# Kernel tuning notes

Hardware: AMD Instinct MI355X
Metric: run time of the kernel (lower is better)

The kernel has to match this reference:

```python
import jax, jax.numpy as jnp
import numpy as np

N = 50000        # num nodes
E = 1600000      # num edges (avg degree 32)
DIN = 128        # dim_in
DOUT = 256       # dim_out
DA = 32          # dim_atten
SLOPE = 0.2      # leaky_relu negative slope


def setup_inputs() -> dict:
    key = jax.random.key(0)
    ks = jax.random.split(key, 9)
    x = jax.random.normal(ks[0], (N, DIN), dtype=jnp.float32)
    row = jax.random.randint(ks[1], (E,), 0, N, dtype=jnp.int32)
    col = jax.random.randint(ks[2], (E,), 0, N, dtype=jnp.int32)
    adj_val = jax.random.uniform(ks[3], (E,), dtype=jnp.float32)
    # learned params (Linear weights stored as [in, out] for x @ W)
    W_row = (jax.random.normal(ks[4], (DIN, DA)) / np.sqrt(DIN)).astype(jnp.float32)
    W_col = (jax.random.normal(ks[5], (DIN, DA)) / np.sqrt(DIN)).astype(jnp.float32)
    W_x = (jax.random.normal(ks[6], (DIN, DOUT)) / np.sqrt(DIN)).astype(jnp.float32)
    b_x = jnp.zeros((DOUT,), dtype=jnp.float32)
    return {"x": x, "row": row, "col": col, "adj_val": adj_val,
            "W_row": W_row, "W_col": W_col, "W_x": W_x, "b_x": b_x}


def reference(x, row, col, adj_val, W_row, W_col, W_x, b_x):
    # per-node attention projections
    a_row = x @ W_row                      # [N, DA]
    a_col = x @ W_col                      # [N, DA]
    # 'Multiply' attention: per-edge dot product scaled by rsqrt(DA)
    atten = jnp.sum(a_row[row] * a_col[col], axis=1) * jax.lax.rsqrt(jnp.float32(DA))  # [E]
    atten = jnp.where(atten >= 0, atten, SLOPE * atten)   # leaky_relu
    atten = jnp.exp(atten - jnp.max(atten))               # global-max-shifted exp
    # row-sum normalization (segment softmax denominator)
    deg = jax.ops.segment_sum(atten, row, num_segments=N)  # [N]
    atten = atten * (1.0 / (deg + 1e-15))[row]             # [E]
    # atten_combine == 'plus': average with original adjacency values
    vals = (adj_val + atten) * 0.5                         # [E]
    # sparse-dense matmul: out[i] = sum_{e: row[e]==i} vals[e] * x[col[e]]
    out = jax.ops.segment_sum(vals[:, None] * x[col], row, num_segments=N)  # [N, DIN]
    return out @ W_x + b_x                                 # [N, DOUT]
```

## Files before the change

kernel.cpp:

```cpp
#include <hip/hip_runtime.h>


#define DIN   128
#define DOUT  256
#define DA    32
#define SLOPE 0.2f
#define RSQRT_DA 0.17677669529663687f
#define BSH   7
#define NBMAX 512
#define BH_CHUNK 8192
#define PB_CHUNK 8192

typedef unsigned int uint;
typedef unsigned short ushort;
typedef __attribute__((ext_vector_type(8))) short bf16x8;
typedef __attribute__((ext_vector_type(4))) float f32x4;

static __device__ __forceinline__ ushort f2bf(float f) {
  const uint u = __float_as_uint(f);
  return (ushort)((u + 0x7fffu + ((u >> 16) & 1u)) >> 16);
}

__global__ __launch_bounds__(256) void wconv_kernel(
    const float* __restrict__ Wx, ushort* __restrict__ wxt,
    const float* __restrict__ Wr, const float* __restrict__ Wc,
    ushort* __restrict__ wrct, int* __restrict__ bcnt, int nb) {
  __shared__ ushort s[16][DIN];
  const int t = threadIdx.x;
  const int b = blockIdx.x;
  if (b < 16) {
    const int c0 = b * 16;
#pragma unroll
    for (int u = 0; u < 8; ++u) {
      const int k = u * 16 + (t >> 4);
      s[t & 15][k] = f2bf(Wx[(size_t)k * DOUT + c0 + (t & 15)]);
    }
    __syncthreads();
    const int c = t >> 4;
    const int kk = (t & 15) * 8;
    *(uint4*)(wxt + (size_t)(c0 + c) * DIN + kk) = *(const uint4*)&s[c][kk];
  } else if (b < 20) {
    const int c = (b - 16) * 16 + (t >> 4);
    const int k0 = (t & 15) * 8;
    const float* src = (c < DA) ? (Wr + c) : (Wc + (c - DA));
    ushort h[8];
#pragma unroll
    for (int j = 0; j < 8; ++j) h[j] = f2bf(src[(size_t)(k0 + j) * DA]);
    uint4 v;
    v.x = (uint)h[0] | ((uint)h[1] << 16);
    v.y = (uint)h[2] | ((uint)h[3] << 16);
    v.z = (uint)h[4] | ((uint)h[5] << 16);
    v.w = (uint)h[6] | ((uint)h[7] << 16);
    *(uint4*)(wrct + (size_t)c * DIN + k0) = v;
  } else {
    for (int i = t; i < nb; i += 256) bcnt[i] = 0;
  }
}

__global__ __launch_bounds__(256) void proj_kernel(
    const float* __restrict__ x, const ushort* __restrict__ wrct,
    float* __restrict__ a_row, ushort* __restrict__ a_colh,
    ushort* __restrict__ xh) {
  __shared__ ushort xb[16][136];
  const int t = threadIdx.x;
  const int node0 = blockIdx.x * 16;
  const float4* xg = (const float4*)(x + (size_t)node0 * DIN);
#pragma unroll
  for (int u = 0; u < 2; ++u) {
    const int f = t + u * 256;
    const float4 v = xg[f];
    ushort4 h;
    h.x = f2bf(v.x); h.y = f2bf(v.y); h.z = f2bf(v.z); h.w = f2bf(v.w);
    *(ushort4*)&xb[f >> 5][(f & 31) * 4] = h;
    ((ushort4*)(xh + (size_t)node0 * DIN))[f] = h;
  }
  __syncthreads();

  const int w = t >> 6;
  const int l = t & 63;
  const int lr = l & 15;
  const int lk = (l >> 4) * 8;
  f32x4 acc = {0.f, 0.f, 0.f, 0.f};
#pragma unroll
  for (int kk = 0; kk < 4; ++kk) {
    const bf16x8 a = *(const bf16x8*)&xb[lr][kk * 32 + lk];
    const bf16x8 bb =
        *(const bf16x8*)(wrct + (size_t)(w * 16 + lr) * DIN + kk * 32 + lk);
    acc = __builtin_amdgcn_mfma_f32_16x16x32_bf16(a, bb, acc, 0, 0, 0);
  }
  const int col = w * 16 + lr;
  const int r0 = (l >> 4) * 4;
#pragma unroll
  for (int r = 0; r < 4; ++r) {
    const int node = node0 + r0 + r;
    if (col < DA)
      a_row[(size_t)node * DA + col] = acc[r] * RSQRT_DA;
    else
      a_colh[(size_t)node * DA + (col - DA)] = f2bf(acc[r]);
  }
}

__global__ __launch_bounds__(512) void bhist_kernel(
    const int* __restrict__ row, int* __restrict__ bcnt, int nb, int E) {
  __shared__ int hist[NBMAX];
  const int t = threadIdx.x;
  for (int b = t; b < nb; b += 512) hist[b] = 0;
  __syncthreads();
  const int e0 = blockIdx.x * BH_CHUNK;
  for (int u = 0; u < BH_CHUNK / 512; ++u) {
    const int e = e0 + u * 512 + t;
    if (e < E) atomicAdd(&hist[row[e] >> BSH], 1);
  }
  __syncthreads();
  for (int b = t; b < nb; b += 512) {
    const int c = hist[b];
    if (c) atomicAdd(&bcnt[b], c);
  }
}

__global__ __launch_bounds__(512) void bscan_kernel(
    const int* __restrict__ bcnt, int* __restrict__ bstart,
    int* __restrict__ bcursor, int nb) {
  __shared__ int s[512];
  const int t = threadIdx.x;
  const int v = (t < nb) ? bcnt[t] : 0;
  s[t] = v;
  __syncthreads();
  for (int ofs = 1; ofs < 512; ofs <<= 1) {
    const int tmp = (t >= ofs) ? s[t - ofs] : 0;
    __syncthreads();
    s[t] += tmp;
    __syncthreads();
  }
  if (t < nb) {
    const int ex = s[t] - v;
    bstart[t] = ex;
    bcursor[t] = ex;
  }
  if (t == nb) bstart[nb] = s[nb - 1];
}

__global__ __launch_bounds__(512) void part_kernel(
    const int* __restrict__ row, const int* __restrict__ col,
    const float* __restrict__ adj, int* __restrict__ bcursor,
    int2* __restrict__ ibuf, int nb, int E) {
  __shared__ int hist[NBMAX];
  __shared__ int base[NBMAX];
  const int t = threadIdx.x;
  const int e0 = blockIdx.x * PB_CHUNK;
  for (int b = t; b < nb; b += 512) hist[b] = 0;
  __syncthreads();
  for (int u = 0; u < PB_CHUNK / 512; ++u) {
    const int e = e0 + u * 512 + t;
    if (e < E) atomicAdd(&hist[row[e] >> BSH], 1);
  }
  __syncthreads();
  for (int b = t; b < nb; b += 512) {
    const int c = hist[b];
    base[b] = c ? atomicAdd(&bcursor[b], c) : 0;
    hist[b] = 0;
  }
  __syncthreads();
  for (int u = 0; u < PB_CHUNK / 512; ++u) {
    const int e = e0 + u * 512 + t;
    if (e < E) {
      const int r = row[e];
      const int b = r >> BSH;
      const int pos = base[b] + atomicAdd(&hist[b], 1);
      ibuf[pos] = make_int2(((r & 127) << 16) | col[e], __float_as_int(adj[e]));
    }
  }
}

__global__ __launch_bounds__(512) void csr_kernel(
    const int* __restrict__ bstart, const int2* __restrict__ ibuf,
    int* __restrict__ off, int2* __restrict__ pk, int n, int E) {
  __shared__ int cnt[128];
  __shared__ int excl[128];
  const int b = blockIdx.x;
  const int t = threadIdx.x;
  const int estart = bstart[b];
  const int eend = bstart[b + 1];
  if (t < 128) cnt[t] = 0;
  __syncthreads();
  for (int e = estart + t; e < eend; e += 512)
    atomicAdd(&cnt[ibuf[e].x >> 16], 1);
  __syncthreads();
  if (t < 128) excl[t] = cnt[t];
  __syncthreads();
  for (int ofs = 1; ofs < 128; ofs <<= 1) {
    const int v = (t < 128 && t >= ofs) ? excl[t - ofs] : 0;
    __syncthreads();
    if (t < 128) excl[t] += v;
    __syncthreads();
  }
  if (t < 128) excl[t] -= cnt[t];
  __syncthreads();
  const int node0 = b << BSH;
  if (t < 128 && node0 + t < n) off[node0 + t] = estart + excl[t];
  if (b == gridDim.x - 1 && t == 0) off[n] = E;
  if (t < 128) cnt[t] = 0;
  __syncthreads();
  for (int e = estart + t; e < eend; e += 512) {
    const int2 v = ibuf[e];
    const int rl = v.x >> 16;
    const int pos = estart + excl[rl] + atomicAdd(&cnt[rl], 1);
    pk[pos] = make_int2(v.x & 0xffff, v.y);
  }
}

#define NODE_BODY(J)                                                    \
  {                                                                     \
    const int2 e = spk[w][half][(J)];                                   \
    const float pv = sp[w][half][(J)];                                  \
    const uint2 xv = xh2[(size_t)e.x * 32 + la];                        \
    const float av = __int_as_float(e.y);                               \
    const float f0 = __uint_as_float(xv.x << 16);                       \
    const float f1 = __uint_as_float(xv.x & 0xffff0000u);               \
    const float f2 = __uint_as_float(xv.y << 16);                       \
    const float f3 = __uint_as_float(xv.y & 0xffff0000u);               \
    aa0 += av * f0; aa1 += av * f1; aa2 += av * f2; aa3 += av * f3;     \
    ap0 += pv * f0; ap1 += pv * f1; ap2 += pv * f2; ap3 += pv * f3;     \
    deg += pv;                                                          \
  }

__global__ __launch_bounds__(256) void node_kernel(
    const uint* __restrict__ xh, const float* __restrict__ a_row,
    const ushort* __restrict__ a_colh, const int* __restrict__ off,
    const int2* __restrict__ pk, ushort* __restrict__ feath, int n) {
  __shared__ int2  spk[4][2][32];
  __shared__ float sp[4][2][32];
  __shared__ float s_ar[4][2][32];
  const int t = threadIdx.x;
  const int w = t >> 6;
  const int lane = t & 63;
  const int half = lane >> 5;
  const int la = lane & 31;
  const int i0 = blockIdx.x * 8 + w * 2;
  if (i0 >= n) return;
  const int i = i0 + half;
  s_ar[w][half][la] = (i < n) ? a_row[(size_t)i * DA + la] : 0.f;
  const int o0 = off[i0];
  const int o1 = off[i0 + 1];
  const int o2 = (i0 + 2 <= n) ? off[i0 + 2] : o1;
  const int d0 = o1 - o0, d1 = o2 - o1;
  const int myoff = half ? o1 : o0;
  const int myd = half ? d1 : d0;
  const int dmax = max(d0, d1);
  const uint2* xh2 = (const uint2*)xh;

  float aa0 = 0.f, aa1 = 0.f, aa2 = 0.f, aa3 = 0.f;
  float ap0 = 0.f, ap1 = 0.f, ap2 = 0.f, ap3 = 0.f;
  float deg = 0.f;

  for (int base = 0; base < dmax; base += 32) {
    const int m = myd - base;
    if (la < m) {
      const int2 e = pk[myoff + base + la];
      spk[w][half][la] = e;
      const uint4* ac = (const uint4*)(a_colh + (size_t)e.x * DA);
      const float* ar = s_ar[w][half];
      float dot = 0.f;
#pragma unroll
      for (int k = 0; k < 4; ++k) {
        const uint4 q = ac[k];
        const float* a = ar + k * 8;
        dot += __uint_as_float(q.x << 16) * a[0] +
               __uint_as_float(q.x & 0xffff0000u) * a[1] +
               __uint_as_float(q.y << 16) * a[2] +
               __uint_as_float(q.y & 0xffff0000u) * a[3] +
               __uint_as_float(q.z << 16) * a[4] +
               __uint_as_float(q.z & 0xffff0000u) * a[5] +
               __uint_as_float(q.w << 16) * a[6] +
               __uint_as_float(q.w & 0xffff0000u) * a[7];
      }
      const float lg = (dot >= 0.f) ? dot : SLOPE * dot;
      sp[w][half][la] = __expf(lg);
    } else {
      spk[w][half][la] = make_int2(0, 0);
      sp[w][half][la] = 0.f;
    }
    const int mmax = min(32, dmax - base);
    int j = 0;
    for (; j + 8 <= mmax; j += 8) {
#pragma unroll
      for (int u = 0; u < 8; ++u) NODE_BODY(j + u)
    }
    for (; j < mmax; ++j) NODE_BODY(j)
  }
  if (i < n) {
    const float inv = 0.5f / (deg + 1e-15f);
    ushort4 h;
    h.x = f2bf(0.5f * aa0 + inv * ap0);
    h.y = f2bf(0.5f * aa1 + inv * ap1);
    h.z = f2bf(0.5f * aa2 + inv * ap2);
    h.w = f2bf(0.5f * aa3 + inv * ap3);
    *(ushort4*)(feath + (size_t)i * DIN + la * 4) = h;
  }
}

__global__ __launch_bounds__(256) void gemm_kernel(
    const ushort* __restrict__ feath, const ushort* __restrict__ wxt,
    const float* __restrict__ bx, float* __restrict__ out) {
  const int t = threadIdx.x;
  const int w = t >> 6;
  const int l = t & 63;
  const int row0 = blockIdx.x * 16;
  const int lr = l & 15;
  const int lk = (l >> 4) * 8;
  const int col0 = w * 64;

  f32x4 acc[4] = {f32x4{0.f, 0.f, 0.f, 0.f}, f32x4{0.f, 0.f, 0.f, 0.f},
                  f32x4{0.f, 0.f, 0.f, 0.f}, f32x4{0.f, 0.f, 0.f, 0.f}};
  const ushort* Abase = feath + (size_t)(row0 + lr) * DIN + lk;
#pragma unroll
  for (int kk = 0; kk < 4; ++kk) {
    const bf16x8 a = *(const bf16x8*)(Abase + kk * 32);
#pragma unroll
    for (int ct = 0; ct < 4; ++ct) {
      const bf16x8 b =
          *(const bf16x8*)(wxt + (size_t)(col0 + ct * 16 + lr) * DIN + kk * 32 + lk);
      acc[ct] = __builtin_amdgcn_mfma_f32_16x16x32_bf16(a, b, acc[ct], 0, 0, 0);
    }
  }
  const int crow0 = row0 + (l >> 4) * 4;
#pragma unroll
  for (int ct = 0; ct < 4; ++ct) {
    const int c = col0 + ct * 16 + lr;
    const float bv = bx[c];
#pragma unroll
    for (int r = 0; r < 4; ++r)
      out[(size_t)(crow0 + r) * DOUT + c] = acc[ct][r] + bv;
  }
}

extern "C" void kernel_launch(void* const* d_in, const int* in_sizes, int n_in,
                              void* d_out, int out_size, void* d_ws, size_t ws_size,
                              hipStream_t stream) {
  const float* x   = (const float*)d_in[0];
  const int*   row = (const int*)d_in[1];
  const int*   col = (const int*)d_in[2];
  const float* adj = (const float*)d_in[3];
  const float* Wr  = (const float*)d_in[4];
  const float* Wc  = (const float*)d_in[5];
  const float* Wx  = (const float*)d_in[6];
  const float* bx  = (const float*)d_in[7];
  float* out = (float*)d_out;

  const int n = in_sizes[0] / DIN;
  const int E = in_sizes[1];
  const int nb = (n + 127) >> BSH;

  int* w4 = (int*)d_ws;
  float* a_row   = (float*)w4;  w4 += (size_t)n * DA;
  ushort* feath  = (ushort*)w4; w4 += (size_t)n * DIN / 2;
  int2*  ibuf    = (int2*)feath;
  int*   off     = w4;          w4 += n + 1;
  int*   bcnt    = w4;          w4 += nb;
  int*   bstart  = w4;          w4 += nb + 1;
  int*   bcursor = w4;          w4 += nb;
  w4 = (int*)(((uintptr_t)w4 + 15) & ~(uintptr_t)15);
  ushort* a_colh = (ushort*)w4; w4 += (size_t)n * DA / 2;
  uint*   xh     = (uint*)w4;   w4 += (size_t)n * DIN / 2;
  int2*   pk     = (int2*)w4;   w4 += (size_t)E * 2;
  ushort* wxt    = (ushort*)w4; w4 += (size_t)DOUT * DIN / 2;
  ushort* wrct   = (ushort*)w4;

  wconv_kernel<<<21, 256, 0, stream>>>(Wx, wxt, Wr, Wc, wrct, bcnt, nb);
  proj_kernel<<<n / 16, 256, 0, stream>>>(x, wrct, a_row, a_colh, (ushort*)xh);
  bhist_kernel<<<(E + BH_CHUNK - 1) / BH_CHUNK, 512, 0, stream>>>(row, bcnt, nb, E);
  bscan_kernel<<<1, 512, 0, stream>>>(bcnt, bstart, bcursor, nb);
  part_kernel<<<(E + PB_CHUNK - 1) / PB_CHUNK, 512, 0, stream>>>(
      row, col, adj, bcursor, ibuf, nb, E);
  csr_kernel<<<nb, 512, 0, stream>>>(bstart, ibuf, off, pk, n, E);
  node_kernel<<<(n + 7) / 8, 256, 0, stream>>>(
      (const uint*)xh, a_row, a_colh, off, pk, feath, n);
  gemm_kernel<<<n / 16, 256, 0, stream>>>(feath, wxt, bx, out);
}
```

Baseline: 295.9 us.

## Replace histogram/scan/CSR passes with fixed-capacity buckets and in-block CSR sort

Drops the bucket histogram, scan and CSR-build kernels. Each bucket of 64 rows now gets a fixed slot of 2560 edges, with padded cursors initialised by wconv. The node kernel loads its bucket's edges into shared memory, counting-sorts them by local row, then processes its 64 nodes in a loop. This removes two extra passes over the edge list and several launches. In exchange, any bucket holding more than 2560 edges overflows silently, and the node kernel runs far fewer, larger blocks with more shared memory, which may cut latency hiding for the gathers.

```diff
diff --git a/kernel.cpp b/kernel.cpp
--- a/kernel.cpp
+++ b/kernel.cpp
@@ -6,9 +6,10 @@
 #define DA    32
 #define SLOPE 0.2f
 #define RSQRT_DA 0.17677669529663687f
-#define BSH   7
-#define NBMAX 512
-#define BH_CHUNK 8192
+#define BSH   6
+#define BCAP  2560
+#define CSTRIDE 32
+#define NBMAX 800
 #define PB_CHUNK 8192
 
 typedef unsigned int uint;
@@ -24,7 +25,7 @@
 __global__ __launch_bounds__(256) void wconv_kernel(
     const float* __restrict__ Wx, ushort* __restrict__ wxt,
     const float* __restrict__ Wr, const float* __restrict__ Wc,
-    ushort* __restrict__ wrct, int* __restrict__ bcnt, int nb) {
+    ushort* __restrict__ wrct, int* __restrict__ bcursor, int nb) {
   __shared__ ushort s[16][DIN];
   const int t = threadIdx.x;
   const int b = blockIdx.x;
@@ -53,7 +54,7 @@
     v.w = (uint)h[6] | ((uint)h[7] << 16);
     *(uint4*)(wrct + (size_t)c * DIN + k0) = v;
   } else {
-    for (int i = t; i < nb; i += 256) bcnt[i] = 0;
+    for (int i = t; i < nb; i += 256) bcursor[i * CSTRIDE] = i * BCAP;
   }
 }
 
@@ -100,46 +101,6 @@
   }
 }
 
-__global__ __launch_bounds__(512) void bhist_kernel(
-    const int* __restrict__ row, int* __restrict__ bcnt, int nb, int E) {
-  __shared__ int hist[NBMAX];
-  const int t = threadIdx.x;
-  for (int b = t; b < nb; b += 512) hist[b] = 0;
-  __syncthreads();
-  const int e0 = blockIdx.x * BH_CHUNK;
-  for (int u = 0; u < BH_CHUNK / 512; ++u) {
-    const int e = e0 + u * 512 + t;
-    if (e < E) atomicAdd(&hist[row[e] >> BSH], 1);
-  }
-  __syncthreads();
-  for (int b = t; b < nb; b += 512) {
-    const int c = hist[b];
-    if (c) atomicAdd(&bcnt[b], c);
-  }
-}
-
-__global__ __launch_bounds__(512) void bscan_kernel(
-    const int* __restrict__ bcnt, int* __restrict__ bstart,
-    int* __restrict__ bcursor, int nb) {
-  __shared__ int s[512];
-  const int t = threadIdx.x;
-  const int v = (t < nb) ? bcnt[t] : 0;
-  s[t] = v;
-  __syncthreads();
-  for (int ofs = 1; ofs < 512; ofs <<= 1) {
-    const int tmp = (t >= ofs) ? s[t - ofs] : 0;
-    __syncthreads();
-    s[t] += tmp;
-    __syncthreads();
-  }
-  if (t < nb) {
-    const int ex = s[t] - v;
-    bstart[t] = ex;
-    bcursor[t] = ex;
-  }
-  if (t == nb) bstart[nb] = s[nb - 1];
-}
-
 __global__ __launch_bounds__(512) void part_kernel(
     const int* __restrict__ row, const int* __restrict__ col,
     const float* __restrict__ adj, int* __restrict__ bcursor,
@@ -157,7 +118,7 @@
   __syncthreads();
   for (int b = t; b < nb; b += 512) {
     const int c = hist[b];
-    base[b] = c ? atomicAdd(&bcursor[b], c) : 0;
+    base[b] = c ? atomicAdd(&bcursor[b * CSTRIDE], c) : 0;
     hist[b] = 0;
   }
   __syncthreads();
@@ -167,45 +128,8 @@
       const int r = row[e];
       const int b = r >> BSH;
       const int pos = base[b] + atomicAdd(&hist[b], 1);
-      ibuf[pos] = make_int2(((r & 127) << 16) | col[e], __float_as_int(adj[e]));
-    }
-  }
-}
-
-__global__ __launch_bounds__(512) void csr_kernel(
-    const int* __restrict__ bstart, const int2* __restrict__ ibuf,
-    int* __restrict__ off, int2* __restrict__ pk, int n, int E) {
-  __shared__ int cnt[128];
-  __shared__ int excl[128];
-  const int b = blockIdx.x;
-  const int t = threadIdx.x;
-  const int estart = bstart[b];
-  const int eend = bstart[b + 1];
-  if (t < 128) cnt[t] = 0;
-  __syncthreads();
-  for (int e = estart + t; e < eend; e += 512)
-    atomicAdd(&cnt[ibuf[e].x >> 16], 1);
-  __syncthreads();
-  if (t < 128) excl[t] = cnt[t];
-  __syncthreads();
-  for (int ofs = 1; ofs < 128; ofs <<= 1) {
-    const int v = (t < 128 && t >= ofs) ? excl[t - ofs] : 0;
-    __syncthreads();
-    if (t < 128) excl[t] += v;
-    __syncthreads();
-  }
-  if (t < 128) excl[t] -= cnt[t];
-  __syncthreads();
-  const int node0 = b << BSH;
-  if (t < 128 && node0 + t < n) off[node0 + t] = estart + excl[t];
-  if (b == gridDim.x - 1 && t == 0) off[n] = E;
-  if (t < 128) cnt[t] = 0;
-  __syncthreads();
-  for (int e = estart + t; e < eend; e += 512) {
-    const int2 v = ibuf[e];
-    const int rl = v.x >> 16;
-    const int pos = estart + excl[rl] + atomicAdd(&cnt[rl], 1);
-    pk[pos] = make_int2(v.x & 0xffff, v.y);
+      ibuf[pos] = make_int2(((r & 63) << 16) | col[e], __float_as_int(adj[e]));
+    }
   }
 }
 
@@ -226,76 +150,124 @@
 
 __global__ __launch_bounds__(256) void node_kernel(
     const uint* __restrict__ xh, const float* __restrict__ a_row,
-    const ushort* __restrict__ a_colh, const int* __restrict__ off,
-    const int2* __restrict__ pk, ushort* __restrict__ feath, int n) {
+    const ushort* __restrict__ a_colh, const int* __restrict__ bcursor,
+    const int2* __restrict__ ibuf, ushort* __restrict__ feath, int n) {
+  __shared__ int2  eL[BCAP];
+  __shared__ int   cnt[64];
+  __shared__ int   excl[65];
   __shared__ int2  spk[4][2][32];
   __shared__ float sp[4][2][32];
   __shared__ float s_ar[4][2][32];
   const int t = threadIdx.x;
+  const int b = blockIdx.x;
+  const int node0 = b << BSH;
+  const int estart = b * BCAP;
+  const int ecnt = bcursor[b * CSTRIDE] - estart;
+
+  if (t < 64) cnt[t] = 0;
+  __syncthreads();
+  int2 myv[BCAP / 256];
+#pragma unroll
+  for (int u = 0; u < BCAP / 256; ++u) {
+    const int e = u * 256 + t;
+    if (e < ecnt) {
+      myv[u] = ibuf[estart + e];
+      atomicAdd(&cnt[myv[u].x >> 16], 1);
+    }
+  }
+  __syncthreads();
+  if (t < 64) excl[t] = cnt[t];
+  __syncthreads();
+  for (int ofs = 1; ofs < 64; ofs <<= 1) {
+    const int v = (t < 64 && t >= ofs) ? excl[t - ofs] : 0;
+    __syncthreads();
+    if (t < 64) excl[t] += v;
+    __syncthreads();
+  }
+  if (t < 64) {
+    const int inc = excl[t];
+    if (t == 63) excl[64] = inc;
+    excl[t] = inc - cnt[t];
+    cnt[t] = 0;
+  }
+  __syncthreads();
+#pragma unroll
+  for (int u = 0; u < BCAP / 256; ++u) {
+    const int e = u * 256 + t;
+    if (e < ecnt) {
+      const int rl = myv[u].x >> 16;
+      const int pos = excl[rl] + atomicAdd(&cnt[rl], 1);
+      eL[pos] = make_int2(myv[u].x & 0xffff, myv[u].y);
+    }
+  }
+  __syncthreads();
+
   const int w = t >> 6;
   const int lane = t & 63;
   const int half = lane >> 5;
   const int la = lane & 31;
-  const int i0 = blockIdx.x * 8 + w * 2;
-  if (i0 >= n) return;
-  const int i = i0 + half;
-  s_ar[w][half][la] = (i < n) ? a_row[(size_t)i * DA + la] : 0.f;
-  const int o0 = off[i0];
-  const int o1 = off[i0 + 1];
-  const int o2 = (i0 + 2 <= n) ? off[i0 + 2] : o1;
-  const int d0 = o1 - o0, d1 = o2 - o1;
-  const int myoff = half ? o1 : o0;
-  const int myd = half ? d1 : d0;
-  const int dmax = max(d0, d1);
   const uint2* xh2 = (const uint2*)xh;
 
-  float aa0 = 0.f, aa1 = 0.f, aa2 = 0.f, aa3 = 0.f;
-  float ap0 = 0.f, ap1 = 0.f, ap2 = 0.f, ap3 = 0.f;
-  float deg = 0.f;
-
-  for (int base = 0; base < dmax; base += 32) {
-    const int m = myd - base;
-    if (la < m) {
-      const int2 e = pk[myoff + base + la];
-      spk[w][half][la] = e;
-      const uint4* ac = (const uint4*)(a_colh + (size_t)e.x * DA);
-      const float* ar = s_ar[w][half];
-      float dot = 0.f;
-#pragma unroll
-      for (int k = 0; k < 4; ++k) {
-        const uint4 q = ac[k];
-        const float* a = ar + k * 8;
-        dot += __uint_as_float(q.x << 16) * a[0] +
-               __uint_as_float(q.x & 0xffff0000u) * a[1] +
-               __uint_as_float(q.y << 16) * a[2] +
-               __uint_as_float(q.y & 0xffff0000u) * a[3] +
-               __uint_as_float(q.z << 16) * a[4] +
-               __uint_as_float(q.z & 0xffff0000u) * a[5] +
-               __uint_as_float(q.w << 16) * a[6] +
-               __uint_as_float(q.w & 0xffff0000u) * a[7];
+  for (int pp = 0; pp < 8; ++pp) {
+    const int rl0 = (pp * 4 + w) * 2;
+    const int i = node0 + rl0 + half;
+    const int o0 = excl[rl0];
+    const int o1 = excl[rl0 + 1];
+    const int o2 = excl[rl0 + 2];
+    const int d0 = o1 - o0, d1 = o2 - o1;
+    const int myoff = half ? o1 : o0;
+    const int myd = half ? d1 : d0;
+    const int dmax = max(d0, d1);
+    s_ar[w][half][la] = (i < n) ? a_row[(size_t)i * DA + la] : 0.f;
+
+    float aa0 = 0.f, aa1 = 0.f, aa2 = 0.f, aa3 = 0.f;
+    float ap0 = 0.f, ap1 = 0.f, ap2 = 0.f, ap3 = 0.f;
+    float deg = 0.f;
+
+    for (int base = 0; base < dmax; base += 32) {
+      const int m = myd - base;
+      if (la < m) {
+        const int2 e = eL[myoff + base + la];
+        spk[w][half][la] = e;
+        const uint4* ac = (const uint4*)(a_colh + (size_t)e.x * DA);
+        const float* ar = s_ar[w][half];
+        float dot = 0.f;
+#pragma unroll
+        for (int k = 0; k < 4; ++k) {
+          const uint4 q = ac[k];
+          const float* a = ar + k * 8;
+          dot += __uint_as_float(q.x << 16) * a[0] +
+                 __uint_as_float(q.x & 0xffff0000u) * a[1] +
+                 __uint_as_float(q.y << 16) * a[2] +
+                 __uint_as_float(q.y & 0xffff0000u) * a[3] +
+                 __uint_as_float(q.z << 16) * a[4] +
+                 __uint_as_float(q.z & 0xffff0000u) * a[5] +
+                 __uint_as_float(q.w << 16) * a[6] +
+                 __uint_as_float(q.w & 0xffff0000u) * a[7];
+        }
+        const float lg = (dot >= 0.f) ? dot : SLOPE * dot;
+        sp[w][half][la] = __expf(lg);
+      } else {
+        spk[w][half][la] = make_int2(0, 0);
+        sp[w][half][la] = 0.f;
       }
-      const float lg = (dot >= 0.f) ? dot : SLOPE * dot;
-      sp[w][half][la] = __expf(lg);
-    } else {
-      spk[w][half][la] = make_int2(0, 0);
-      sp[w][half][la] = 0.f;
-    }
-    const int mmax = min(32, dmax - base);
-    int j = 0;
-    for (; j + 8 <= mmax; j += 8) {
-#pragma unroll
-      for (int u = 0; u < 8; ++u) NODE_BODY(j + u)
-    }
-    for (; j < mmax; ++j) NODE_BODY(j)
-  }
-  if (i < n) {
-    const float inv = 0.5f / (deg + 1e-15f);
-    ushort4 h;
-    h.x = f2bf(0.5f * aa0 + inv * ap0);
-    h.y = f2bf(0.5f * aa1 + inv * ap1);
-    h.z = f2bf(0.5f * aa2 + inv * ap2);
-    h.w = f2bf(0.5f * aa3 + inv * ap3);
-    *(ushort4*)(feath + (size_t)i * DIN + la * 4) = h;
+      const int mmax = min(32, dmax - base);
+      int j = 0;
+      for (; j + 8 <= mmax; j += 8) {
+#pragma unroll
+        for (int u = 0; u < 8; ++u) NODE_BODY(j + u)
+      }
+      for (; j < mmax; ++j) NODE_BODY(j)
+    }
+    if (i < n) {
+      const float inv = 0.5f / (deg + 1e-15f);
+      ushort4 h;
+      h.x = f2bf(0.5f * aa0 + inv * ap0);
+      h.y = f2bf(0.5f * aa1 + inv * ap1);
+      h.z = f2bf(0.5f * aa2 + inv * ap2);
+      h.w = f2bf(0.5f * aa3 + inv * ap3);
+      *(ushort4*)(feath + (size_t)i * DIN + la * 4) = h;
+    }
   }
 }
 
@@ -349,31 +321,23 @@
 
   const int n = in_sizes[0] / DIN;
   const int E = in_sizes[1];
-  const int nb = (n + 127) >> BSH;
+  const int nb = (n + 63) >> BSH;
 
   int* w4 = (int*)d_ws;
   float* a_row   = (float*)w4;  w4 += (size_t)n * DA;
   ushort* feath  = (ushort*)w4; w4 += (size_t)n * DIN / 2;
-  int2*  ibuf    = (int2*)feath;
-  int*   off     = w4;          w4 += n + 1;
-  int*   bcnt    = w4;          w4 += nb;
-  int*   bstart  = w4;          w4 += nb + 1;
-  int*   bcursor = w4;          w4 += nb;
-  w4 = (int*)(((uintptr_t)w4 + 15) & ~(uintptr_t)15);
   ushort* a_colh = (ushort*)w4; w4 += (size_t)n * DA / 2;
   uint*   xh     = (uint*)w4;   w4 += (size_t)n * DIN / 2;
-  int2*   pk     = (int2*)w4;   w4 += (size_t)E * 2;
+  int2*   ibuf   = (int2*)w4;   w4 += (size_t)nb * BCAP * 2;
+  int*    bcursor= w4;          w4 += (size_t)nb * CSTRIDE;
   ushort* wxt    = (ushort*)w4; w4 += (size_t)DOUT * DIN / 2;
   ushort* wrct   = (ushort*)w4;
 
-  wconv_kernel<<<21, 256, 0, stream>>>(Wx, wxt, Wr, Wc, wrct, bcnt, nb);
+  wconv_kernel<<<21, 256, 0, stream>>>(Wx, wxt, Wr, Wc, wrct, bcursor, nb);
   proj_kernel<<<n / 16, 256, 0, stream>>>(x, wrct, a_row, a_colh, (ushort*)xh);
-  bhist_kernel<<<(E + BH_CHUNK - 1) / BH_CHUNK, 512, 0, stream>>>(row, bcnt, nb, E);
-  bscan_kernel<<<1, 512, 0, stream>>>(bcnt, bstart, bcursor, nb);
   part_kernel<<<(E + PB_CHUNK - 1) / PB_CHUNK, 512, 0, stream>>>(
       row, col, adj, bcursor, ibuf, nb, E);
-  csr_kernel<<<nb, 512, 0, stream>>>(bstart, ibuf, off, pk, n, E);
-  node_kernel<<<(n + 7) / 8, 256, 0, stream>>>(
-      (const uint*)xh, a_row, a_colh, off, pk, feath, n);
+  node_kernel<<<nb, 256, 0, stream>>>(
+      (const uint*)xh, a_row, a_colh, bcursor, ibuf, feath, n);
   gemm_kernel<<<n / 16, 256, 0, stream>>>(feath, wxt, bx, out);
 }
```

Result: faster. 260.9 us (-11.8%).
